# Optimization experiments

Hardware: AMD Instinct MI355X
Metric: run time of the kernel (lower is better)

## Reference

```python
import jax, jax.numpy as jnp
import numpy as np

BEAM = 4
START = 1


def setup_inputs() -> dict:
    key = jax.random.key(0)
    ks = jax.random.split(key, 10)
    S, B, H, E, V = 32, 16, 1024, 256, 32000
    Din = E + E + H  # embed + enc_input_step + enc_output_step
    sc = 0.02
    return {
        "enc_h_n": jax.random.normal(ks[0], (1, B, H), jnp.float32),
        "enc_c_n": jax.random.normal(ks[1], (1, B, H), jnp.float32),
        "enc_outputs": jax.random.normal(ks[2], (S, B, H), jnp.float32),
        "enc_inputs": jax.random.normal(ks[3], (S, B, E), jnp.float32),
        "embed": jax.random.normal(ks[4], (V, E), jnp.float32) * sc,
        "w_ih": jax.random.normal(ks[5], (Din, 4 * H), jnp.float32) * sc,
        "w_hh": jax.random.normal(ks[6], (H, 4 * H), jnp.float32) * sc,
        "b_lstm": jnp.zeros((4 * H,), jnp.float32),
        "w_out": jax.random.normal(ks[7], (H, V), jnp.float32) * sc,
        "b_out": jnp.zeros((V,), jnp.float32),
    }


def reference(enc_h_n, enc_c_n, enc_outputs, enc_inputs,
              embed, w_ih, w_hh, b_lstm, w_out, b_out):
    S, B, _ = enc_inputs.shape
    H = enc_h_n.shape[2]
    V = w_out.shape[1]
    K = BEAM

    def decode(word, h, c, ein, eout):
        # word: [B] int, h/c: [B,H], ein: [B,E], eout: [B,H]
        x = jnp.concatenate([embed[word], ein, eout], axis=-1)  # [B,Din]
        gates = x @ w_ih + h @ w_hh + b_lstm                    # [B,4H]
        i, f, g, o = jnp.split(gates, 4, axis=-1)
        c2 = jax.nn.sigmoid(f) * c + jax.nn.sigmoid(i) * jnp.tanh(g)
        h2 = jax.nn.sigmoid(o) * jnp.tanh(c2)
        logits = h2 @ w_out + b_out                             # [B,V]
        return logits, h2, c2

    # ---- init_beam_search (step 0) ----
    h0, c0 = enc_h_n[0], enc_c_n[0]
    word0 = jnp.full((B,), START, dtype=jnp.int32)
    logits0, h1, c1 = decode(word0, h0, c0, enc_inputs[0], enc_outputs[0])
    probs0 = jax.nn.softmax(logits0, axis=-1)
    top_v, top_i = jax.lax.top_k(probs0, K)  # [B,K]
    # NOTE: original code never updates current_scores inside the loop -> constant
    scores = top_v

    h = jnp.broadcast_to(h1, (K, B, H)) + 0.0  # per-beam hidden state copies
    c = jnp.broadcast_to(c1, (K, B, H)) + 0.0
    word = top_i  # [B,K]

    decode_beams = jax.vmap(decode, in_axes=(1, 0, 0, None, None))

    def step(carry, xs):
        h, c, word = carry
        ein, eout = xs
        logits, h2, c2 = decode_beams(word, h, c, ein, eout)  # [K,B,V]
        probs = jax.nn.softmax(logits, axis=-1)
        # space_search layout: beam b occupies cols [b*V, (b+1)*V); tile repeats
        # each beam score V times -> equivalent to broadcast over vocab axis.
        space = jnp.transpose(probs, (1, 0, 2)) * scores[:, :, None]  # [B,K,V]
        _, ti = jax.lax.top_k(space.reshape(B, K * V), K)             # [B,K]
        word2 = ti % V
        return (h2, c2, word2), ti

    (_, _, _), tis = jax.lax.scan(step, (h, c, word),
                                  (enc_inputs[1:], enc_outputs[1:]))
    out = jnp.concatenate([top_i[None], tis], axis=0)  # [S,B,K]
    return jnp.transpose(out, (2, 1, 0)).astype(jnp.int32)  # [K,B,S]
```

## Files before the change

kernel.cpp:

```cpp
#include <hip/hip_runtime.h>
#include <math.h>

#define S_LEN 32
#define B_N   16
#define H_N   1024
#define E_N   256
#define V_N   32000
#define KBEAM 4
#define DIN   1536
#define D2    2560
#define R_N   64
#define NDS   20
#define GKS   4
#define NB    500

typedef _Float16 f16;
typedef f16   f16x8 __attribute__((ext_vector_type(8)));
typedef float f32x4 __attribute__((ext_vector_type(4)));
#define MFMA(A,B,C) __builtin_amdgcn_mfma_f32_16x16x32_f16(A,B,C,0,0,0)

__device__ __forceinline__ float sigmf(float x){ return 1.0f/(1.0f+expf(-x)); }
__device__ __forceinline__ bool better(float v1,int i1,float v2,int i2){
  return (v1>v2) || (v1==v2 && i1<i2);
}
__device__ __forceinline__ void ins4(float bv,int bi,
    float&av0,float&av1,float&av2,float&av3,int&ai0,int&ai1,int&ai2,int&ai3){
  if (better(bv,bi,av3,ai3)){ av3=bv; ai3=bi;
    if (better(av3,ai3,av2,ai2)){ float t=av2;av2=av3;av3=t; int q=ai2;ai2=ai3;ai3=q;
      if (better(av2,ai2,av1,ai1)){ t=av1;av1=av2;av2=t; q=ai1;ai1=ai2;ai2=q;
        if (better(av1,ai1,av0,ai0)){ t=av0;av0=av1;av1=t; q=ai0;ai0=ai1;ai1=q; } } } }
}

__device__ __forceinline__ void packx(f16* xpk, int r, int k, float v){
  int m = r >> 4, lm = r & 15;
  int ks = k >> 5, kq = (k & 31) >> 3, i = k & 7;
  int l = lm + 16*kq;
  size_t base = (((size_t)m*80 + ks)*2)*512 + l*8 + i;
  f16 hh = (f16)v;
  xpk[base]       = hh;
  xpk[base + 512] = (f16)((v - (float)hh)*4096.0f);
}

#define FMA16(w4, h4) { \
  acc[0][0]=fmaf(w4.x,h4.x,acc[0][0]); acc[0][1]=fmaf(w4.x,h4.y,acc[0][1]); \
  acc[0][2]=fmaf(w4.x,h4.z,acc[0][2]); acc[0][3]=fmaf(w4.x,h4.w,acc[0][3]); \
  acc[1][0]=fmaf(w4.y,h4.x,acc[1][0]); acc[1][1]=fmaf(w4.y,h4.y,acc[1][1]); \
  acc[1][2]=fmaf(w4.y,h4.z,acc[1][2]); acc[1][3]=fmaf(w4.y,h4.w,acc[1][3]); \
  acc[2][0]=fmaf(w4.z,h4.x,acc[2][0]); acc[2][1]=fmaf(w4.z,h4.y,acc[2][1]); \
  acc[2][2]=fmaf(w4.z,h4.z,acc[2][2]); acc[2][3]=fmaf(w4.z,h4.w,acc[2][3]); \
  acc[3][0]=fmaf(w4.w,h4.x,acc[3][0]); acc[3][1]=fmaf(w4.w,h4.y,acc[3][1]); \
  acc[3][2]=fmaf(w4.w,h4.z,acc[3][2]); acc[3][3]=fmaf(w4.w,h4.w,acc[3][3]); }

#define LOADSET(S, s) { size_t o_ = (size_t)(s)*1024; \
  Bh##S  = *(const f16x8*)(wp + o_);  Bl##S  = *(const f16x8*)(wp + o_ + 512); \
  A0h##S = *(const f16x8*)(hp0 + o_); A0l##S = *(const f16x8*)(hp0 + o_ + 512); \
  A1h##S = *(const f16x8*)(hp1 + o_); A1l##S = *(const f16x8*)(hp1 + o_ + 512); \
  A2h##S = *(const f16x8*)(hp2 + o_); A2l##S = *(const f16x8*)(hp2 + o_ + 512); \
  A3h##S = *(const f16x8*)(hp3 + o_); A3l##S = *(const f16x8*)(hp3 + o_ + 512); }
#define COMPSET(S) { \
  c10 = MFMA(A0h##S, Bh##S, c10); c20 = MFMA(A0l##S, Bh##S, c20); c20 = MFMA(A0h##S, Bl##S, c20); \
  c11 = MFMA(A1h##S, Bh##S, c11); c21 = MFMA(A1l##S, Bh##S, c21); c21 = MFMA(A1h##S, Bl##S, c21); \
  c12 = MFMA(A2h##S, Bh##S, c12); c22 = MFMA(A2l##S, Bh##S, c22); c22 = MFMA(A2h##S, Bl##S, c22); \
  c13 = MFMA(A3h##S, Bh##S, c13); c23 = MFMA(A3l##S, Bh##S, c23); c23 = MFMA(A3h##S, Bl##S, c23); }
#define DECLFRAGS \
  f32x4 c10={0,0,0,0}, c11={0,0,0,0}, c12={0,0,0,0}, c13={0,0,0,0}; \
  f32x4 c20={0,0,0,0}, c21={0,0,0,0}, c22={0,0,0,0}, c23={0,0,0,0}; \
  f16x8 Bh0,Bl0,A0h0,A1h0,A2h0,A3h0,A0l0,A1l0,A2l0,A3l0; \
  f16x8 Bh1,Bl1,A0h1,A1h1,A2h1,A3h1,A0l1,A1l1,A2l1,A3l1;

__global__ __launch_bounds__(256) void k_init(
    const float* __restrict__ enc_h_n, const float* __restrict__ enc_c_n,
    const float* __restrict__ enc_outputs, const float* __restrict__ enc_inputs,
    const float* __restrict__ embed, float* __restrict__ x, float* __restrict__ c,
    f16* __restrict__ xpk){
  int r = blockIdx.x, tid = threadIdx.x, b = r & 15;
  float* xr = x + (size_t)r*D2;
  float v0 = embed[E_N + tid];
  float v1 = enc_inputs[b*E_N + tid];
  xr[tid]       = v0;
  xr[E_N + tid] = v1;
  float eo[4], hh[4];
  #pragma unroll
  for (int q=0;q<4;++q){
    eo[q] = enc_outputs[b*H_N + q*256 + tid];
    hh[q] = enc_h_n[b*H_N + q*256 + tid];
    xr[2*E_N + q*256 + tid] = eo[q];
    xr[DIN + q*256 + tid]   = hh[q];
    c[(size_t)r*H_N + q*256 + tid] = enc_c_n[b*H_N + q*256 + tid];
  }
  if (xpk){
    packx(xpk, r, tid, v0);
    packx(xpk, r, E_N + tid, v1);
    #pragma unroll
    for (int q=0;q<4;++q){
      packx(xpk, r, 2*E_N + q*256 + tid, eo[q]);
      packx(xpk, r, DIN + q*256 + tid,   hh[q]);
    }
  }
}

__global__ __launch_bounds__(256) void k_convw(
    const float* __restrict__ w, f16* __restrict__ wpk){
  __shared__ f16 Th[64][66];
  __shared__ f16 Tl[64][66];
  int v0 = blockIdx.x*64, d0 = blockIdx.y*64;
  int tid = threadIdx.x;
  int r = tid >> 4, cq = (tid & 15)*4;
  #pragma unroll
  for (int rr=0; rr<4; ++rr){
    int d = r + rr*16;
    float4 x = *(const float4*)&w[(size_t)(d0+d)*V_N + v0 + cq];
    f16 h;
    h=(f16)x.x; Th[d][cq+0]=h; Tl[d][cq+0]=(f16)((x.x-(float)h)*4096.0f);
    h=(f16)x.y; Th[d][cq+1]=h; Tl[d][cq+1]=(f16)((x.y-(float)h)*4096.0f);
    h=(f16)x.z; Th[d][cq+2]=h; Tl[d][cq+2]=(f16)((x.z-(float)h)*4096.0f);
    h=(f16)x.w; Th[d][cq+3]=h; Tl[d][cq+3]=(f16)((x.w-(float)h)*4096.0f);
  }
  __syncthreads();
  int T2 = tid >> 6, l = tid & 63;
  int lm = l & 15, kq = l >> 4;
  int Tg = blockIdx.x*4 + T2;
  #pragma unroll
  for (int ks2=0; ks2<2; ++ks2){
    int ksg = blockIdx.y*2 + ks2;
    f16x8 a, b2;
    #pragma unroll
    for (int i=0;i<8;++i){
      int dd = ks2*32 + kq*8 + i;
      a[i]  = Th[dd][T2*16 + lm];
      b2[i] = Tl[dd][T2*16 + lm];
    }
    size_t base = ((size_t)(Tg*32 + ksg)*2)*512 + l*8;
    *(f16x8*)&wpk[base]       = a;
    *(f16x8*)&wpk[base + 512] = b2;
  }
}

__global__ __launch_bounds__(256) void k_convg(
    const float* __restrict__ w_ih, const float* __restrict__ w_hh,
    f16* __restrict__ wgpk){
  __shared__ f16 Th[64][66];
  __shared__ f16 Tl[64][66];
  int c0 = blockIdx.x*64, k0 = blockIdx.y*64;
  int tid = threadIdx.x;
  int r = tid >> 4, cq = (tid & 15)*4;
  #pragma unroll
  for (int rr=0; rr<4; ++rr){
    int d = r + rr*16;
    int row = k0 + d;
    const float* src = (row < DIN) ? &w_ih[(size_t)row*4096 + c0 + cq]
                                   : &w_hh[(size_t)(row-DIN)*4096 + c0 + cq];
    float4 x = *(const float4*)src;
    f16 h;
    h=(f16)x.x; Th[d][cq+0]=h; Tl[d][cq+0]=(f16)((x.x-(float)h)*4096.0f);
    h=(f16)x.y; Th[d][cq+1]=h; Tl[d][cq+1]=(f16)((x.y-(float)h)*4096.0f);
    h=(f16)x.z; Th[d][cq+2]=h; Tl[d][cq+2]=(f16)((x.z-(float)h)*4096.0f);
    h=(f16)x.w; Th[d][cq+3]=h; Tl[d][cq+3]=(f16)((x.w-(float)h)*4096.0f);
  }
  __syncthreads();
  int T2 = tid >> 6, l = tid & 63;
  int lm = l & 15, kq = l >> 4;
  int Tg = blockIdx.x*4 + T2;
  #pragma unroll
  for (int ks2=0; ks2<2; ++ks2){
    int ksg = blockIdx.y*2 + ks2;
    f16x8 a, b2;
    #pragma unroll
    for (int i=0;i<8;++i){
      int dd = ks2*32 + kq*8 + i;
      a[i]  = Th[dd][T2*16 + lm];
      b2[i] = Tl[dd][T2*16 + lm];
    }
    size_t base = (((size_t)Tg*80 + ksg)*2)*512 + l*8;
    *(f16x8*)&wgpk[base]       = a;
    *(f16x8*)&wgpk[base + 512] = b2;
  }
}

__global__ __launch_bounds__(256) void k_gates_mfma(
    const f16* __restrict__ wgpk, const f16* __restrict__ xpk,
    float* __restrict__ gpart){
  int tid = threadIdx.x;
  int lane = tid & 63;
  int wv = tid >> 6;
  int T  = blockIdx.x*4 + wv;
  int ksb = blockIdx.y*20;

  const f16* wp  = wgpk + (((size_t)T*80 + ksb)*2)*512 + lane*8;
  const f16* hp0 = xpk + (((size_t)0*80 + ksb)*2)*512 + lane*8;
  const f16* hp1 = xpk + (((size_t)1*80 + ksb)*2)*512 + lane*8;
  const f16* hp2 = xpk + (((size_t)2*80 + ksb)*2)*512 + lane*8;
  const f16* hp3 = xpk + (((size_t)3*80 + ksb)*2)*512 + lane*8;

  DECLFRAGS

  LOADSET(0, 0)
  for (int s=0; s<20; s+=2){
    LOADSET(1, s+1)
    COMPSET(0)
    if (s+2<20) LOADSET(0, s+2)
    COMPSET(1)
  }

  const float inv = 1.0f/4096.0f;
  int lm = lane & 15;
  int rb = (lane>>4)*4;
  int col = T*16 + lm;
  size_t rbase = (size_t)blockIdx.y*R_N;
#define GSTT(mt, A1, A2) { \
  _Pragma("unroll") for (int rg=0; rg<4; ++rg){ \
    gpart[(rbase + (mt)*16 + rb + rg)*4096 + col] = A1[rg] + A2[rg]*inv; } }
  GSTT(0, c10, c20) GSTT(1, c11, c21) GSTT(2, c12, c22) GSTT(3, c13, c23)
}

#define GWLD(d, off) (*(const float4*)((((d) < DIN) ? (w_ih + (size_t)(d)*4096) \
                       : (w_hh + (size_t)((d)-DIN)*4096)) + (off)))
__global__ __launch_bounds__(256) void k_gates(
    const float* __restrict__ x, const float* __restrict__ w_ih,
    const float* __restrict__ w_hh, float* __restrict__ gpart){
  int tid = threadIdx.x;
  int jt = blockIdx.x, ks = blockIdx.y;
  int cx = tid & 15, ry = tid >> 4;
  int cb = jt*64;
  int wdd = tid >> 4, wseg = tid & 15;
  int xrow = tid >> 3, xseg = tid & 7;

  __shared__ float Wt0[32][64], Wt1[32][64];
  __shared__ float Xt0[32][68], Xt1[32][68];

  float acc[4][4];
  #pragma unroll
  for (int cc=0;cc<4;++cc)
    #pragma unroll
    for (int rr=0;rr<4;++rr) acc[cc][rr]=0.f;

  int d0 = ks*128;
  const float* xp0 = x + (size_t)xrow*D2 + d0 + xseg*4;
  const float* xp1 = x + (size_t)(xrow+32)*D2 + d0 + xseg*4;

#define GLQ(WA,WB,X0,X1, ch) { int d_ = d0 + (ch)*32; \
  WA = GWLD(d_+wdd,    cb+wseg*4); \
  WB = GWLD(d_+16+wdd, cb+wseg*4); \
  X0 = *(const float4*)(xp0 + (ch)*32); \
  X1 = *(const float4*)(xp1 + (ch)*32); }
#define GSQ(Wt,Xt, WA,WB,X0,X1) { \
  *(float4*)&Wt[wdd][wseg*4]    = WA; \
  *(float4*)&Wt[wdd+16][wseg*4] = WB; \
  Xt[xseg*4+0][xrow] = X0.x; Xt[xseg*4+1][xrow] = X0.y; \
  Xt[xseg*4+2][xrow] = X0.z; Xt[xseg*4+3][xrow] = X0.w; \
  Xt[xseg*4+0][xrow+32] = X1.x; Xt[xseg*4+1][xrow+32] = X1.y; \
  Xt[xseg*4+2][xrow+32] = X1.z; Xt[xseg*4+3][xrow+32] = X1.w; }
#define GCQ(Wt,Xt) { _Pragma("unroll 8") for (int dd=0; dd<32; ++dd){ \
    float4 w4 = *(const float4*)&Wt[dd][cx*4]; \
    float4 h4 = *(const float4*)&Xt[dd][ry*4]; \
    FMA16(w4, h4) } }

  float4 wA0,wB0,x00,x10, wA1,wB1,x01,x11;
  GLQ(wA0,wB0,x00,x10, 0)
  GSQ(Wt0,Xt0, wA0,wB0,x00,x10)
  GLQ(wA1,wB1,x01,x11, 1)
  __syncthreads();

  for (int ch=0; ch<4; ch+=2){
    if (ch+2<4) GLQ(wA0,wB0,x00,x10, ch+2)
    GSQ(Wt1,Xt1, wA1,wB1,x01,x11)
    GCQ(Wt0,Xt0)
    __syncthreads();
    if (ch+3<4) GLQ(wA1,wB1,x01,x11, ch+3)
    if (ch+2<4) GSQ(Wt0,Xt0, wA0,wB0,x00,x10)
    GCQ(Wt1,Xt1)
    if (ch+2<4) __syncthreads();
  }
  #pragma unroll
  for (int rr=0;rr<4;++rr){
    float4 o; o.x=acc[0][rr]; o.y=acc[1][rr]; o.z=acc[2][rr]; o.w=acc[3][rr];
    *(float4*)&gpart[((size_t)(ks*R_N + ry*4+rr))*4096 + cb + cx*4] = o;
  }
}

__global__ __launch_bounds__(256) void k_lstm(
    const float* __restrict__ gpart, const float* __restrict__ b_lstm,
    float* __restrict__ c, float* __restrict__ xn, float* __restrict__ h2t,
    f16* __restrict__ hpk, f16* __restrict__ xpk, int nds){
  int r = blockIdx.x, tid = threadIdx.x;
  int j = blockIdx.y*256 + tid;
  float gi = b_lstm[j], gf = b_lstm[1024+j], gg = b_lstm[2048+j], go = b_lstm[3072+j];
  for (int ds=0; ds<nds; ++ds){
    size_t base = ((size_t)ds*R_N + r)*4096;
    gi += gpart[base + j];      gf += gpart[base + 1024 + j];
    gg += gpart[base + 2048+j]; go += gpart[base + 3072 + j];
  }
  float cv = c[(size_t)r*H_N + j];
  float c2 = sigmf(gf)*cv + sigmf(gi)*tanhf(gg);
  float h2 = sigmf(go)*tanhf(c2);
  c[(size_t)r*H_N + j] = c2;
  if (hpk){
    f16 hh = (f16)h2;
    int m = r >> 4, lm = r & 15;
    int ks = j >> 5, kq = (j & 31) >> 3, i = j & 7;
    int l = lm + 16*kq;
    size_t base2 = ((size_t)(m*32 + ks)*2)*512 + l*8 + i;
    hpk[base2]       = hh;
    hpk[base2 + 512] = (f16)((h2 - (float)hh)*4096.0f);
    packx(xpk, r, DIN + j, h2);
  } else {
    xn[(size_t)r*D2 + DIN + j] = h2;
    h2t[(size_t)j*R_N + r] = h2;
  }
}

__global__ __launch_bounds__(256) void k_logits_mfma(
    const f16* __restrict__ wpk, const f16* __restrict__ hpk,
    const float* __restrict__ b_out,
    float* __restrict__ pm, float* __restrict__ pz,
    float* __restrict__ pv, int* __restrict__ pi){
  int tid = threadIdx.x;
  int lane = tid & 63;
  int wv = tid >> 6;
  int T  = blockIdx.x*4 + wv;
  int vb = T*16;

  const f16* wp  = wpk + ((size_t)(T*32))*2*512 + lane*8;
  const f16* hp0 = hpk + ((size_t)(0*32))*2*512 + lane*8;
  const f16* hp1 = hpk + ((size_t)(1*32))*2*512 + lane*8;
  const f16* hp2 = hpk + ((size_t)(2*32))*2*512 + lane*8;
  const f16* hp3 = hpk + ((size_t)(3*32))*2*512 + lane*8;

  DECLFRAGS

  LOADSET(0, 0)
  for (int s=0; s<32; s+=2){
    LOADSET(1, s+1)
    COMPSET(0)
    if (s+2<32) LOADSET(0, s+2)
    COMPSET(1)
  }

  __shared__ float Ls[64][68];

  const float inv = 1.0f/4096.0f;
  int lm = lane & 15;
  int rb = (lane>>4)*4;
  float bias = b_out[vb + lm];
#define STT(mt, A1, A2) { \
  _Pragma("unroll") for (int rg=0; rg<4; ++rg){ \
    Ls[(mt)*16 + rb + rg][wv*16 + lm] = A1[rg] + A2[rg]*inv + bias; } }
  STT(0, c10, c20) STT(1, c11, c21) STT(2, c12, c22) STT(3, c13, c23)
  __syncthreads();

  int cx = tid & 15, ry = tid >> 4;
  int cb = blockIdx.x * 64;
  #pragma unroll
  for (int rr=0;rr<4;++rr){
    int row = ry*4 + rr;
    float v0 = Ls[row][cx*4+0], v1 = Ls[row][cx*4+1];
    float v2 = Ls[row][cx*4+2], v3 = Ls[row][cx*4+3];
    int   c0i = cb + cx*4;
    float tv0=-INFINITY,tv1=-INFINITY,tv2=-INFINITY,tv3=-INFINITY;
    int   ti0=0x7fffffff,ti1=0x7fffffff,ti2=0x7fffffff,ti3=0x7fffffff;
    ins4(v0,c0i+0,tv0,tv1,tv2,tv3,ti0,ti1,ti2,ti3);
    ins4(v1,c0i+1,tv0,tv1,tv2,tv3,ti0,ti1,ti2,ti3);
    ins4(v2,c0i+2,tv0,tv1,tv2,tv3,ti0,ti1,ti2,ti3);
    ins4(v3,c0i+3,tv0,tv1,tv2,tv3,ti0,ti1,ti2,ti3);
    float z = expf(v0-tv0)+expf(v1-tv0)+expf(v2-tv0)+expf(v3-tv0);
    #pragma unroll
    for (int msk=1; msk<16; msk<<=1){
      float om  = __shfl_xor(tv0, msk, 16);
      float oz  = __shfl_xor(z,   msk, 16);
      float ov1 = __shfl_xor(tv1, msk, 16);
      float ov2 = __shfl_xor(tv2, msk, 16);
      float ov3 = __shfl_xor(tv3, msk, 16);
      int   oi0 = __shfl_xor(ti0, msk, 16);
      int   oi1 = __shfl_xor(ti1, msk, 16);
      int   oi2 = __shfl_xor(ti2, msk, 16);
      int   oi3 = __shfl_xor(ti3, msk, 16);
      float M = fmaxf(tv0, om);
      z = z*expf(tv0-M) + oz*expf(om-M);
      ins4(om, oi0, tv0,tv1,tv2,tv3, ti0,ti1,ti2,ti3);
      ins4(ov1,oi1, tv0,tv1,tv2,tv3, ti0,ti1,ti2,ti3);
      ins4(ov2,oi2, tv0,tv1,tv2,tv3, ti0,ti1,ti2,ti3);
      ins4(ov3,oi3, tv0,tv1,tv2,tv3, ti0,ti1,ti2,ti3);
    }
    if (cx == 0){
      size_t base = (size_t)row*NB + blockIdx.x;
      pm[base]=tv0; pz[base]=z;
      pv[base*4+0]=tv0; pv[base*4+1]=tv1; pv[base*4+2]=tv2; pv[base*4+3]=tv3;
      pi[base*4+0]=ti0; pi[base*4+1]=ti1; pi[base*4+2]=ti2; pi[base*4+3]=ti3;
    }
  }
}

__global__ __launch_bounds__(256) void k_logits_fused(
    const float* __restrict__ h2t, const float* __restrict__ w_out,
    const float* __restrict__ b_out,
    float* __restrict__ pm, float* __restrict__ pz,
    float* __restrict__ pv, int* __restrict__ pi){
  int tid = threadIdx.x;
  int cx  = tid & 15, ry = tid >> 4;
  int cb  = blockIdx.x * 64;
  int sdd = tid >> 4, seg = tid & 15;
  __shared__ float Wt[32][64];
  __shared__ float Ht[32][64];
  float acc[4][4];
  #pragma unroll
  for (int cc=0;cc<4;++cc)
    #pragma unroll
    for (int rr=0;rr<4;++rr) acc[cc][rr]=0.f;
  const float* gW = w_out + (size_t)sdd*V_N + cb + seg*4;
  const float* gH = h2t + sdd*64 + seg*4;
#define FLQ(WA,WB,HA,HB, ch) { \
  const float* gWn = gW + (size_t)(ch)*32*V_N; \
  const float* gHn = gH + (size_t)(ch)*32*64; \
  WA = *(const float4*)gWn; WB = *(const float4*)(gWn + (size_t)16*V_N); \
  HA = *(const float4*)gHn; HB = *(const float4*)(gHn + 16*64); }
#define FSQ(WA,WB,HA,HB) { \
  *(float4*)&Wt[sdd][seg*4]    = WA; \
  *(float4*)&Wt[sdd+16][seg*4] = WB; \
  *(float4*)&Ht[sdd][seg*4]    = HA; \
  *(float4*)&Ht[sdd+16][seg*4] = HB; }
#define FCQ() { _Pragma("unroll 8") for (int dd=0; dd<32; ++dd){ \
    float4 w4 = *(const float4*)&Wt[dd][cx*4]; \
    float4 h4 = *(const float4*)&Ht[dd][ry*4]; \
    FMA16(w4, h4) } }
  float4 wA0,wB0,hA0,hB0, wA1,wB1,hA1,hB1;
  FLQ(wA0,wB0,hA0,hB0, 0)
  FSQ(wA0,wB0,hA0,hB0)
  FLQ(wA1,wB1,hA1,hB1, 1)
  __syncthreads();
  for (int ch=0; ch<32; ch+=2){
    if (ch+2<32) FLQ(wA0,wB0,hA0,hB0, ch+2)
    FCQ()
    __syncthreads();
    FSQ(wA1,wB1,hA1,hB1)
    __syncthreads();
    if (ch+3<32) FLQ(wA1,wB1,hA1,hB1, ch+3)
    FCQ()
    if (ch+2<32){
      __syncthreads();
      FSQ(wA0,wB0,hA0,hB0)
      __syncthreads();
    }
  }
  float4 bias = *(const float4*)&b_out[cb + cx*4];
  #pragma unroll
  for (int rr=0;rr<4;++rr){
    float v0 = acc[0][rr]+bias.x, v1 = acc[1][rr]+bias.y;
    float v2 = acc[2][rr]+bias.z, v3 = acc[3][rr]+bias.w;
    int   c0i = cb + cx*4;
    float tv0=-INFINITY,tv1=-INFINITY,tv2=-INFINITY,tv3=-INFINITY;
    int   ti0=0x7fffffff,ti1=0x7fffffff,ti2=0x7fffffff,ti3=0x7fffffff;
    ins4(v0,c0i+0,tv0,tv1,tv2,tv3,ti0,ti1,ti2,ti3);
    ins4(v1,c0i+1,tv0,tv1,tv2,tv3,ti0,ti1,ti2,ti3);
    ins4(v2,c0i+2,tv0,tv1,tv2,tv3,ti0,ti1,ti2,ti3);
    ins4(v3,c0i+3,tv0,tv1,tv2,tv3,ti0,ti1,ti2,ti3);
    float z = expf(v0-tv0)+expf(v1-tv0)+expf(v2-tv0)+expf(v3-tv0);
    #pragma unroll
    for (int msk=1; msk<16; msk<<=1){
      float om  = __shfl_xor(tv0, msk, 16);
      float oz  = __shfl_xor(z,   msk, 16);
      float ov1 = __shfl_xor(tv1, msk, 16);
      float ov2 = __shfl_xor(tv2, msk, 16);
      float ov3 = __shfl_xor(tv3, msk, 16);
      int   oi0 = __shfl_xor(ti0, msk, 16);
      int   oi1 = __shfl_xor(ti1, msk, 16);
      int   oi2 = __shfl_xor(ti2, msk, 16);
      int   oi3 = __shfl_xor(ti3, msk, 16);
      float M = fmaxf(tv0, om);
      z = z*expf(tv0-M) + oz*expf(om-M);
      ins4(om, oi0, tv0,tv1,tv2,tv3, ti0,ti1,ti2,ti3);
      ins4(ov1,oi1, tv0,tv1,tv2,tv3, ti0,ti1,ti2,ti3);
      ins4(ov2,oi2, tv0,tv1,tv2,tv3, ti0,ti1,ti2,ti3);
      ins4(ov3,oi3, tv0,tv1,tv2,tv3, ti0,ti1,ti2,ti3);
    }
    if (cx == 0){
      int row = ry*4 + rr;
      size_t base = (size_t)row*NB + blockIdx.x;
      pm[base]=tv0; pz[base]=z;
      pv[base*4+0]=tv0; pv[base*4+1]=tv1; pv[base*4+2]=tv2; pv[base*4+3]=tv3;
      pi[base*4+0]=ti0; pi[base*4+1]=ti1; pi[base*4+2]=ti2; pi[base*4+3]=ti3;
    }
  }
}

__global__ __launch_bounds__(256) void k_final(
    const float* __restrict__ pm, const float* __restrict__ pz,
    const float* __restrict__ pv, const int* __restrict__ pi,
    float* __restrict__ scores, int* __restrict__ out, int t,
    float* __restrict__ xn, f16* __restrict__ xpk,
    const float* __restrict__ enc_inputs, const float* __restrict__ enc_outputs,
    const float* __restrict__ embed){
  int b = blockIdx.x, tid = threadIdx.x;
  int kk = tid >> 6, lane = tid & 63;
  __shared__ float fM[KBEAM], fZ[KBEAM], fV[16];
  __shared__ int   fI[16], sw[KBEAM];
  int nk = (t==0) ? 1 : KBEAM;
  if (kk < nk){
    size_t rb = (size_t)(kk*B_N + b)*NB;
    float m=-INFINITY, z=0.f;
    float av0=-INFINITY,av1=-INFINITY,av2=-INFINITY,av3=-INFINITY;
    int   ai0=0x7fffffff,ai1=0x7fffffff,ai2=0x7fffffff,ai3=0x7fffffff;
    for (int p0=lane; p0<NB; p0+=64){
      size_t p = rb + p0;
      float mf = pm[p];
      float M = fmaxf(m, mf);
      z = z*expf(m-M) + pz[p]*expf(mf-M);
      m = M;
      #pragma unroll
      for (int q=0;q<4;++q)
        ins4(pv[p*4+q], pi[p*4+q], av0,av1,av2,av3, ai0,ai1,ai2,ai3);
    }
    #pragma unroll
    for (int msk=1; msk<64; msk<<=1){
      float om  = __shfl_xor(m,   msk);
      float oz  = __shfl_xor(z,   msk);
      float ov0 = __shfl_xor(av0, msk);
      float ov1 = __shfl_xor(av1, msk);
      float ov2 = __shfl_xor(av2, msk);
      float ov3 = __shfl_xor(av3, msk);
      int   oi0 = __shfl_xor(ai0, msk);
      int   oi1 = __shfl_xor(ai1, msk);
      int   oi2 = __shfl_xor(ai2, msk);
      int   oi3 = __shfl_xor(ai3, msk);
      float M = fmaxf(m, om);
      z = z*expf(m-M) + oz*expf(om-M);
      m = M;
      ins4(ov0,oi0, av0,av1,av2,av3, ai0,ai1,ai2,ai3);
      ins4(ov1,oi1, av0,av1,av2,av3, ai0,ai1,ai2,ai3);
      ins4(ov2,oi2, av0,av1,av2,av3, ai0,ai1,ai2,ai3);
      ins4(ov3,oi3, av0,av1,av2,av3, ai0,ai1,ai2,ai3);
    }
    if (lane == 0){
      fM[kk]=m; fZ[kk]=z;
      fV[kk*4+0]=av0; fV[kk*4+1]=av1; fV[kk*4+2]=av2; fV[kk*4+3]=av3;
      fI[kk*4+0]=ai0; fI[kk*4+1]=ai1; fI[kk*4+2]=ai2; fI[kk*4+3]=ai3;
    }
  }
  __syncthreads();
  if (tid==0){
    if (t==0){
      #pragma unroll
      for (int j=0;j<4;++j){
        float p = expf(fV[j]-fM[0])/fZ[0];
        scores[b*4+j] = p;
        out[j*(B_N*S_LEN) + b*S_LEN] = fI[j];
        sw[j] = fI[j];
      }
    } else {
      float cv[16]; int cj[16];
      for (int k=0;k<4;++k){
        float s = scores[b*4+k];
        #pragma unroll
        for (int j=0;j<4;++j){
          cv[k*4+j] = expf(fV[k*4+j]-fM[k])/fZ[k]*s;
          cj[k*4+j] = k*V_N + fI[k*4+j];
        }
      }
      bool used[16];
      for (int i=0;i<16;++i) used[i]=false;
      for (int rank=0;rank<4;++rank){
        int best=-1;
        for (int i=0;i<16;++i){
          if (used[i]) continue;
          if (best<0 || cv[i]>cv[best] || (cv[i]==cv[best] && cj[i]<cj[best])) best=i;
        }
        used[best]=true;
        out[rank*(B_N*S_LEN) + b*S_LEN + t] = cj[best];
        sw[rank] = cj[best] % V_N;
      }
    }
  }
  __syncthreads();
  if (t < S_LEN-1){
    const float* ein = enc_inputs  + (size_t)(t+1)*B_N*E_N + (size_t)b*E_N;
    const float* eo  = enc_outputs + (size_t)(t+1)*B_N*H_N + (size_t)b*H_N;
    #pragma unroll
    for (int j=0;j<KBEAM;++j){
      int r = j*B_N + b;
      const float* em = embed + (size_t)sw[j]*E_N;
      float v0 = em[tid], v1 = ein[tid];
      if (xpk){
        packx(xpk, r, tid, v0); packx(xpk, r, E_N + tid, v1);
        #pragma unroll
        for (int q=0;q<4;++q) packx(xpk, r, 2*E_N + q*256 + tid, eo[q*256 + tid]);
      } else {
        float* xr = xn + (size_t)r*D2;
        xr[tid]       = v0;
        xr[E_N + tid] = v1;
        #pragma unroll
        for (int q=0;q<4;++q) xr[2*E_N + q*256 + tid] = eo[q*256 + tid];
      }
    }
  }
}

extern "C" void kernel_launch(void* const* d_in, const int* in_sizes, int n_in,
                              void* d_out, int out_size, void* d_ws, size_t ws_size,
                              hipStream_t stream) {
  (void)in_sizes; (void)n_in; (void)out_size;
  const float* enc_h_n     = (const float*)d_in[0];
  const float* enc_c_n     = (const float*)d_in[1];
  const float* enc_outputs = (const float*)d_in[2];
  const float* enc_inputs  = (const float*)d_in[3];
  const float* embed       = (const float*)d_in[4];
  const float* w_ih        = (const float*)d_in[5];
  const float* w_hh        = (const float*)d_in[6];
  const float* b_lstm      = (const float*)d_in[7];
  const float* w_out       = (const float*)d_in[8];
  const float* b_out       = (const float*)d_in[9];
  int* out = (int*)d_out;

  float* ws = (float*)d_ws;
  const size_t FRONTF = (size_t)R_N*D2*2 + (size_t)R_N*H_N + (size_t)H_N*R_N;
  const size_t HSPLF  = (size_t)R_N*H_N;
  const size_t XPKF   = (size_t)R_N*D2;
  const size_t GPARTF = (size_t)NDS*R_N*4096;
  const size_t STATF  = (size_t)R_N*NB*10;
  const size_t WSPLF  = (size_t)V_N*H_N;
  const size_t WGPKF  = (size_t)D2*4096;
  size_t need_split = (FRONTF + HSPLF + XPKF + GPARTF + STATF + 64 + WSPLF + WGPKF)*sizeof(float);
  bool use_split = (ws_size >= need_split);

  float* xA     = ws;
  float* xB     = xA + (size_t)R_N*D2;
  float* cbuf   = xB + (size_t)R_N*D2;
  float* h2t    = cbuf + (size_t)R_N*H_N;
  f16*   hpk    = (f16*)(h2t + (size_t)H_N*R_N);
  f16*   xpk    = (f16*)(h2t + (size_t)H_N*R_N + HSPLF);
  float* big    = h2t + (size_t)H_N*R_N + HSPLF + XPKF;
  float* gpart  = big;
  float* pm     = big + GPARTF;
  float* pz     = pm + (size_t)R_N*NB;
  float* pv     = pz + (size_t)R_N*NB;
  int*   pi     = (int*)(pv + (size_t)R_N*NB*4);
  float* scoresb= (float*)(pi + (size_t)R_N*NB*4);
  f16*   wpk    = (f16*)(scoresb + 64);
  f16*   wgpk   = (f16*)((float*)(scoresb + 64) + WSPLF);

  f16* hpk_arg = use_split ? hpk : (f16*)0;
  f16* xpk_arg = use_split ? xpk : (f16*)0;

  if (use_split){
    k_convw<<<dim3(V_N/64, H_N/64), 256, 0, stream>>>(w_out, wpk);
    k_convg<<<dim3(4096/64, D2/64), 256, 0, stream>>>(w_ih, w_hh, wgpk);
  }
  k_init<<<R_N, 256, 0, stream>>>(enc_h_n, enc_c_n, enc_outputs, enc_inputs,
                                  embed, xA, cbuf, xpk_arg);

  for (int t=0; t<S_LEN; ++t){
    float* xc = (t & 1) ? xB : xA;
    float* xn = (t & 1) ? xA : xB;
    if (use_split){
      k_gates_mfma<<<dim3(64, GKS), 256, 0, stream>>>(wgpk, xpk, gpart);
      k_lstm<<<dim3(R_N, 4), 256, 0, stream>>>(gpart, b_lstm, cbuf, xn, h2t,
                                               hpk_arg, xpk_arg, GKS);
      k_logits_mfma<<<NB, 256, 0, stream>>>(wpk, hpk, b_out, pm, pz, pv, pi);
    } else {
      k_gates <<<dim3(64, NDS), 256, 0, stream>>>(xc, w_ih, w_hh, gpart);
      k_lstm<<<dim3(R_N, 4), 256, 0, stream>>>(gpart, b_lstm, cbuf, xn, h2t,
                                               (f16*)0, (f16*)0, NDS);
      k_logits_fused<<<NB, 256, 0, stream>>>(h2t, w_out, b_out, pm, pz, pv, pi);
    }
    k_final <<<B_N, 256, 0, stream>>>(pm, pz, pv, pi, scoresb, out, t, xn, xpk_arg,
                                      enc_inputs, enc_outputs, embed);
  }
}
```

Before: 2.712 ms.

## Fuse gate GEMM and LSTM cell into one kernel with interleaved gate columns

Gate weights are repacked so each 16-column MFMA tile holds the i,f,g,o gates for four hidden units. A new kernel computes all K-splits across four waves, reduces them in shared memory and applies the LSTM cell directly. This replaces the separate gates and lstm kernels and their global gpart round trip. The packed input is double-buffered so the next step's x can be written while the current one is read. The cost is 256 blocks each doing the full K reduction per tile, versus the previous split grid.

```diff
diff --git a/kernel.cpp b/kernel.cpp
--- a/kernel.cpp
+++ b/kernel.cpp
@@ -11,7 +11,6 @@
 #define D2    2560
 #define R_N   64
 #define NDS   20
-#define GKS   4
 #define NB    500
 
 typedef _Float16 f16;
@@ -141,21 +140,22 @@
     f16* __restrict__ wgpk){
   __shared__ f16 Th[64][66];
   __shared__ f16 Tl[64][66];
-  int c0 = blockIdx.x*64, k0 = blockIdx.y*64;
+  int jb = blockIdx.x*16, k0 = blockIdx.y*64;
   int tid = threadIdx.x;
-  int r = tid >> 4, cq = (tid & 15)*4;
+  int r = tid >> 4;
+  int g = (tid & 15) >> 2, q = tid & 3;
   #pragma unroll
   for (int rr=0; rr<4; ++rr){
     int d = r + rr*16;
     int row = k0 + d;
-    const float* src = (row < DIN) ? &w_ih[(size_t)row*4096 + c0 + cq]
-                                   : &w_hh[(size_t)(row-DIN)*4096 + c0 + cq];
+    const float* src = (row < DIN) ? &w_ih[(size_t)row*4096 + g*1024 + jb + q*4]
+                                   : &w_hh[(size_t)(row-DIN)*4096 + g*1024 + jb + q*4];
     float4 x = *(const float4*)src;
     f16 h;
-    h=(f16)x.x; Th[d][cq+0]=h; Tl[d][cq+0]=(f16)((x.x-(float)h)*4096.0f);
-    h=(f16)x.y; Th[d][cq+1]=h; Tl[d][cq+1]=(f16)((x.y-(float)h)*4096.0f);
-    h=(f16)x.z; Th[d][cq+2]=h; Tl[d][cq+2]=(f16)((x.z-(float)h)*4096.0f);
-    h=(f16)x.w; Th[d][cq+3]=h; Tl[d][cq+3]=(f16)((x.w-(float)h)*4096.0f);
+    h=(f16)x.x; Th[d][(q*4+0)*4+g]=h; Tl[d][(q*4+0)*4+g]=(f16)((x.x-(float)h)*4096.0f);
+    h=(f16)x.y; Th[d][(q*4+1)*4+g]=h; Tl[d][(q*4+1)*4+g]=(f16)((x.y-(float)h)*4096.0f);
+    h=(f16)x.z; Th[d][(q*4+2)*4+g]=h; Tl[d][(q*4+2)*4+g]=(f16)((x.z-(float)h)*4096.0f);
+    h=(f16)x.w; Th[d][(q*4+3)*4+g]=h; Tl[d][(q*4+3)*4+g]=(f16)((x.w-(float)h)*4096.0f);
   }
   __syncthreads();
   int T2 = tid >> 6, l = tid & 63;
@@ -177,20 +177,21 @@
   }
 }
 
-__global__ __launch_bounds__(256) void k_gates_mfma(
-    const f16* __restrict__ wgpk, const f16* __restrict__ xpk,
-    float* __restrict__ gpart){
+__global__ __launch_bounds__(256) void k_cell(
+    const f16* __restrict__ wgpk, const f16* __restrict__ xpk_cur,
+    const float* __restrict__ b_lstm, float* __restrict__ c,
+    f16* __restrict__ hpk, f16* __restrict__ xpk_next){
   int tid = threadIdx.x;
   int lane = tid & 63;
   int wv = tid >> 6;
-  int T  = blockIdx.x*4 + wv;
-  int ksb = blockIdx.y*20;
-
-  const f16* wp  = wgpk + (((size_t)T*80 + ksb)*2)*512 + lane*8;
-  const f16* hp0 = xpk + (((size_t)0*80 + ksb)*2)*512 + lane*8;
-  const f16* hp1 = xpk + (((size_t)1*80 + ksb)*2)*512 + lane*8;
-  const f16* hp2 = xpk + (((size_t)2*80 + ksb)*2)*512 + lane*8;
-  const f16* hp3 = xpk + (((size_t)3*80 + ksb)*2)*512 + lane*8;
+  int T  = blockIdx.x;
+  int ksb = wv*20;
+
+  const f16* wp  = wgpk    + (((size_t)T*80 + ksb)*2)*512 + lane*8;
+  const f16* hp0 = xpk_cur + (((size_t)0*80 + ksb)*2)*512 + lane*8;
+  const f16* hp1 = xpk_cur + (((size_t)1*80 + ksb)*2)*512 + lane*8;
+  const f16* hp2 = xpk_cur + (((size_t)2*80 + ksb)*2)*512 + lane*8;
+  const f16* hp3 = xpk_cur + (((size_t)3*80 + ksb)*2)*512 + lane*8;
 
   DECLFRAGS
 
@@ -202,15 +203,36 @@
     COMPSET(1)
   }
 
+  __shared__ float Gs[4][64][17];
   const float inv = 1.0f/4096.0f;
   int lm = lane & 15;
-  int rb = (lane>>4)*4;
-  int col = T*16 + lm;
-  size_t rbase = (size_t)blockIdx.y*R_N;
-#define GSTT(mt, A1, A2) { \
+  int rb2 = (lane>>4)*4;
+#define CSTT(mt, A1, A2) { \
   _Pragma("unroll") for (int rg=0; rg<4; ++rg){ \
-    gpart[(rbase + (mt)*16 + rb + rg)*4096 + col] = A1[rg] + A2[rg]*inv; } }
-  GSTT(0, c10, c20) GSTT(1, c11, c21) GSTT(2, c12, c22) GSTT(3, c13, c23)
+    Gs[wv][(mt)*16 + rb2 + rg][lm] = A1[rg] + A2[rg]*inv; } }
+  CSTT(0, c10, c20) CSTT(1, c11, c21) CSTT(2, c12, c22) CSTT(3, c13, c23)
+  __syncthreads();
+
+  int r = tid >> 2, u = tid & 3;
+  int j = T*4 + u;
+  float gi = Gs[0][r][u*4+0] + Gs[1][r][u*4+0] + Gs[2][r][u*4+0] + Gs[3][r][u*4+0] + b_lstm[j];
+  float gf = Gs[0][r][u*4+1] + Gs[1][r][u*4+1] + Gs[2][r][u*4+1] + Gs[3][r][u*4+1] + b_lstm[1024+j];
+  float gg = Gs[0][r][u*4+2] + Gs[1][r][u*4+2] + Gs[2][r][u*4+2] + Gs[3][r][u*4+2] + b_lstm[2048+j];
+  float go = Gs[0][r][u*4+3] + Gs[1][r][u*4+3] + Gs[2][r][u*4+3] + Gs[3][r][u*4+3] + b_lstm[3072+j];
+  float cv = c[(size_t)r*H_N + j];
+  float c2v = sigmf(gf)*cv + sigmf(gi)*tanhf(gg);
+  float h2 = sigmf(go)*tanhf(c2v);
+  c[(size_t)r*H_N + j] = c2v;
+  {
+    f16 hh = (f16)h2;
+    int m = r >> 4, lmr = r & 15;
+    int ks = j >> 5, kq = (j & 31) >> 3, i2 = j & 7;
+    int l = lmr + 16*kq;
+    size_t b2 = ((size_t)(m*32 + ks)*2)*512 + l*8 + i2;
+    hpk[b2]       = hh;
+    hpk[b2 + 512] = (f16)((h2 - (float)hh)*4096.0f);
+  }
+  packx(xpk_next, r, DIN + j, h2);
 }
 
 #define GWLD(d, off) (*(const float4*)((((d) < DIN) ? (w_ih + (size_t)(d)*4096) \
@@ -281,7 +303,7 @@
 __global__ __launch_bounds__(256) void k_lstm(
     const float* __restrict__ gpart, const float* __restrict__ b_lstm,
     float* __restrict__ c, float* __restrict__ xn, float* __restrict__ h2t,
-    f16* __restrict__ hpk, f16* __restrict__ xpk, int nds){
+    int nds){
   int r = blockIdx.x, tid = threadIdx.x;
   int j = blockIdx.y*256 + tid;
   float gi = b_lstm[j], gf = b_lstm[1024+j], gg = b_lstm[2048+j], go = b_lstm[3072+j];
@@ -294,19 +316,8 @@
   float c2 = sigmf(gf)*cv + sigmf(gi)*tanhf(gg);
   float h2 = sigmf(go)*tanhf(c2);
   c[(size_t)r*H_N + j] = c2;
-  if (hpk){
-    f16 hh = (f16)h2;
-    int m = r >> 4, lm = r & 15;
-    int ks = j >> 5, kq = (j & 31) >> 3, i = j & 7;
-    int l = lm + 16*kq;
-    size_t base2 = ((size_t)(m*32 + ks)*2)*512 + l*8 + i;
-    hpk[base2]       = hh;
-    hpk[base2 + 512] = (f16)((h2 - (float)hh)*4096.0f);
-    packx(xpk, r, DIN + j, h2);
-  } else {
-    xn[(size_t)r*D2 + DIN + j] = h2;
-    h2t[(size_t)j*R_N + r] = h2;
-  }
+  xn[(size_t)r*D2 + DIN + j] = h2;
+  h2t[(size_t)j*R_N + r] = h2;
 }
 
 __global__ __launch_bounds__(256) void k_logits_mfma(
@@ -486,7 +497,7 @@
     const float* __restrict__ pm, const float* __restrict__ pz,
     const float* __restrict__ pv, const int* __restrict__ pi,
     float* __restrict__ scores, int* __restrict__ out, int t,
-    float* __restrict__ xn, f16* __restrict__ xpk,
+    float* __restrict__ xn, f16* __restrict__ xpk_next,
     const float* __restrict__ enc_inputs, const float* __restrict__ enc_outputs,
     const float* __restrict__ embed){
   int b = blockIdx.x, tid = threadIdx.x;
@@ -578,10 +589,10 @@
       int r = j*B_N + b;
       const float* em = embed + (size_t)sw[j]*E_N;
       float v0 = em[tid], v1 = ein[tid];
-      if (xpk){
-        packx(xpk, r, tid, v0); packx(xpk, r, E_N + tid, v1);
+      if (xpk_next){
+        packx(xpk_next, r, tid, v0); packx(xpk_next, r, E_N + tid, v1);
         #pragma unroll
-        for (int q=0;q<4;++q) packx(xpk, r, 2*E_N + q*256 + tid, eo[q*256 + tid]);
+        for (int q=0;q<4;++q) packx(xpk_next, r, 2*E_N + q*256 + tid, eo[q*256 + tid]);
       } else {
         float* xr = xn + (size_t)r*D2;
         xr[tid]       = v0;
@@ -617,7 +628,7 @@
   const size_t STATF  = (size_t)R_N*NB*10;
   const size_t WSPLF  = (size_t)V_N*H_N;
   const size_t WGPKF  = (size_t)D2*4096;
-  size_t need_split = (FRONTF + HSPLF + XPKF + GPARTF + STATF + 64 + WSPLF + WGPKF)*sizeof(float);
+  size_t need_split = (FRONTF + HSPLF + 2*XPKF + GPARTF + STATF + 64 + WSPLF + WGPKF)*sizeof(float);
   bool use_split = (ws_size >= need_split);
 
   float* xA     = ws;
@@ -625,8 +636,9 @@
   float* cbuf   = xB + (size_t)R_N*D2;
   float* h2t    = cbuf + (size_t)R_N*H_N;
   f16*   hpk    = (f16*)(h2t + (size_t)H_N*R_N);
-  f16*   xpk    = (f16*)(h2t + (size_t)H_N*R_N + HSPLF);
-  float* big    = h2t + (size_t)H_N*R_N + HSPLF + XPKF;
+  f16*   xpkA   = (f16*)(h2t + (size_t)H_N*R_N + HSPLF);
+  f16*   xpkB   = (f16*)(h2t + (size_t)H_N*R_N + HSPLF + XPKF);
+  float* big    = h2t + (size_t)H_N*R_N + HSPLF + 2*XPKF;
   float* gpart  = big;
   float* pm     = big + GPARTF;
   float* pz     = pm + (size_t)R_N*NB;
@@ -636,31 +648,29 @@
   f16*   wpk    = (f16*)(scoresb + 64);
   f16*   wgpk   = (f16*)((float*)(scoresb + 64) + WSPLF);
 
-  f16* hpk_arg = use_split ? hpk : (f16*)0;
-  f16* xpk_arg = use_split ? xpk : (f16*)0;
-
   if (use_split){
     k_convw<<<dim3(V_N/64, H_N/64), 256, 0, stream>>>(w_out, wpk);
     k_convg<<<dim3(4096/64, D2/64), 256, 0, stream>>>(w_ih, w_hh, wgpk);
   }
   k_init<<<R_N, 256, 0, stream>>>(enc_h_n, enc_c_n, enc_outputs, enc_inputs,
-                                  embed, xA, cbuf, xpk_arg);
+                                  embed, xA, cbuf, use_split ? xpkA : (f16*)0);
 
   for (int t=0; t<S_LEN; ++t){
     float* xc = (t & 1) ? xB : xA;
     float* xn = (t & 1) ? xA : xB;
+    f16* xpk_cur  = (t & 1) ? xpkB : xpkA;
+    f16* xpk_next = (t & 1) ? xpkA : xpkB;
     if (use_split){
-      k_gates_mfma<<<dim3(64, GKS), 256, 0, stream>>>(wgpk, xpk, gpart);
-      k_lstm<<<dim3(R_N, 4), 256, 0, stream>>>(gpart, b_lstm, cbuf, xn, h2t,
-                                               hpk_arg, xpk_arg, GKS);
+      k_cell<<<256, 256, 0, stream>>>(wgpk, xpk_cur, b_lstm, cbuf, hpk, xpk_next);
       k_logits_mfma<<<NB, 256, 0, stream>>>(wpk, hpk, b_out, pm, pz, pv, pi);
+      k_final<<<B_N, 256, 0, stream>>>(pm, pz, pv, pi, scoresb, out, t, xn, xpk_next,
+                                       enc_inputs, enc_outputs, embed);
     } else {
       k_gates <<<dim3(64, NDS), 256, 0, stream>>>(xc, w_ih, w_hh, gpart);
-      k_lstm<<<dim3(R_N, 4), 256, 0, stream>>>(gpart, b_lstm, cbuf, xn, h2t,
-                                               (f16*)0, (f16*)0, NDS);
+      k_lstm<<<dim3(R_N, 4), 256, 0, stream>>>(gpart, b_lstm, cbuf, xn, h2t, NDS);
       k_logits_fused<<<NB, 256, 0, stream>>>(h2t, w_out, b_out, pm, pz, pv, pi);
-    }
-    k_final <<<B_N, 256, 0, stream>>>(pm, pz, pv, pi, scoresb, out, t, xn, xpk_arg,
-                                      enc_inputs, enc_outputs, embed);
-  }
-}
+      k_final<<<B_N, 256, 0, stream>>>(pm, pz, pv, pi, scoresb, out, t, xn, (f16*)0,
+                                       enc_inputs, enc_outputs, embed);
+    }
+  }
+}
```

Result: no change. 2.714 ms (+0.1%).
